# Kernel tuning notes

Measured on AMD Instinct MI355X. Metric: run time of the kernel, lower is better.

Reference implementation:

```python
import jax, jax.numpy as jnp
import numpy as np

B, C, N = 2, 512, 2048
HEADS, DIM_HEAD, SCALE = 16, 64, 8.0
H_DIM = HEADS * DIM_HEAD
EPS = 1e-12  # F.normalize default eps


def setup_inputs() -> dict:
    key = jax.random.key(0)
    ks = jax.random.split(key, 5)
    x = jax.random.normal(ks[0], (B, C, N), dtype=jnp.float32)
    Wqkv = jax.random.normal(ks[1], (3 * H_DIM, C), dtype=jnp.float32) * (1.0 / np.sqrt(C))
    q_scale = jnp.ones((DIM_HEAD,), dtype=jnp.float32)
    k_scale = jnp.ones((DIM_HEAD,), dtype=jnp.float32)
    Wout = jax.random.normal(ks[2], (C, H_DIM), dtype=jnp.float32) * (1.0 / np.sqrt(H_DIM))
    bout = jax.random.normal(ks[3], (C,), dtype=jnp.float32) * 0.01
    return {"x": x, "Wqkv": Wqkv, "q_scale": q_scale, "k_scale": k_scale,
            "Wout": Wout, "bout": bout}


def _l2norm(t):
    # F.normalize(t, dim=-1): t / max(||t||, eps)
    n = jnp.sqrt(jnp.sum(t * t, axis=-1, keepdims=True))
    return t / jnp.maximum(n, EPS)


def reference(x, Wqkv, q_scale, k_scale, Wout, bout):
    # 1x1 conv == pointwise matmul over channel dim
    qkv = jnp.einsum('oc,bcn->bon', Wqkv, x)              # [B, 3*H_DIM, N]
    q, k, v = jnp.split(qkv, 3, axis=1)
    # unflatten channels -> [B, H, D, N]
    def to_heads(t):
        return t.reshape(B, HEADS, DIM_HEAD, N)
    q, k, v = map(to_heads, (q, k, v))
    # cosine attention: l2-normalize q,k over head dim, apply learned per-dim scales
    q = _l2norm(q.transpose(0, 1, 3, 2)) * q_scale        # [B, H, N, D]
    k = _l2norm(k.transpose(0, 1, 3, 2)) * k_scale        # [B, H, N, D]
    sim = jnp.einsum('bhid,bhjd->bhij', q, k) * SCALE     # [B, H, N, N]
    attn = jax.nn.softmax(sim, axis=-1)
    out = jnp.einsum('bhij,bhdj->bhid', attn, v)          # [B, H, N, D]
    out = out.transpose(0, 1, 3, 2).reshape(B, H_DIM, N)  # b h n d -> b (h d) n
    return jnp.einsum('oc,bcn->bon', Wout, out) + bout[None, :, None]
```

## Files before the change

### kernel.cpp

```cpp
#include <hip/hip_runtime.h>
#include <hip/hip_bf16.h>

#define BATCH 2
#define CCH   512
#define NSEQ  2048
#define HEADS 16
#define DHEAD 64
#define HDIM  1024
#define ODIM  3072
#define QK_PRESCALE 11.541560327111707f

typedef short short4v __attribute__((ext_vector_type(4)));
typedef short short8 __attribute__((ext_vector_type(8)));
typedef float float4v __attribute__((ext_vector_type(4)));
typedef int   int4v   __attribute__((ext_vector_type(4)));

__device__ __forceinline__ unsigned short f2bf(float f) {
    unsigned int u = __float_as_uint(f);
    return (unsigned short)((u + 0x7FFFu + ((u >> 16) & 1u)) >> 16);
}
__device__ __forceinline__ unsigned short f2bf_fast(float f) {
    return (unsigned short)((__float_as_uint(f) + 0x8000u) >> 16);
}
__device__ __forceinline__ float fexp2(float x) {
#if __has_builtin(__builtin_amdgcn_exp2f)
    return __builtin_amdgcn_exp2f(x);
#else
    return exp2f(x);
#endif
}
__device__ __forceinline__ int pack_bf16(float lo, float hi) {
#if __has_builtin(__builtin_amdgcn_cvt_pk_bf16_f32)
    typedef __bf16 bf2_t __attribute__((ext_vector_type(2)));
    bf2_t v = __builtin_amdgcn_cvt_pk_bf16_f32(lo, hi);
    return __builtin_bit_cast(int, v);
#else
    return (int)f2bf_fast(lo) | ((int)(unsigned)f2bf_fast(hi) << 16);
#endif
}

typedef __attribute__((address_space(1))) const void* as1_cvp;
typedef __attribute__((address_space(3))) void* as3_vp;
__device__ __forceinline__ void cp16(const void* g, void* l) {
    __builtin_amdgcn_global_load_lds((as1_cvp)g, (as3_vp)l, 16, 0, 0);
}
__global__ __launch_bounds__(256) void k_prep(
    const float* __restrict__ Wqkv, const float* __restrict__ Wout,
    const float* __restrict__ x,
    const float* __restrict__ qs, const float* __restrict__ ks,
    unsigned short* __restrict__ Wqkvb, unsigned short* __restrict__ Woutb,
    unsigned short* __restrict__ xt, float* __restrict__ M) {
    const int bx = blockIdx.x;
    if (bx < 2048) {
        if (bx == 0 && threadIdx.x < 64) {
            int lane = threadIdx.x;
            float p = fabsf(qs[lane] * ks[lane]);
#pragma unroll
            for (int off = 1; off < 64; off <<= 1) p = fmaxf(p, __shfl_xor(p, off));
            if (lane == 0) *M = QK_PRESCALE * p;
        }
        int i4 = (bx * 256 + threadIdx.x) * 4;
        const float* src; unsigned short* dst; int idx;
        if (i4 < ODIM * CCH) { src = Wqkv; dst = Wqkvb; idx = i4; }
        else { src = Wout; dst = Woutb; idx = i4 - ODIM * CCH; }
        float4 v = *(const float4*)(src + idx);
        ushort4 o;
        o.x = f2bf(v.x); o.y = f2bf(v.y); o.z = f2bf(v.z); o.w = f2bf(v.w);
        *(ushort4*)(dst + idx) = o;
        return;
    }
    __shared__ unsigned short t[64][65];
    const int fx = bx - 2048;
    const int n0 = (fx & 31) * 64;
    const int c0 = ((fx >> 5) & 7) * 64;
    const int b  = fx >> 8;
    const int tr = threadIdx.x >> 6, tc = threadIdx.x & 63;
    const float* xs = x + (size_t)b * CCH * NSEQ;
    unsigned short* xd = xt + (size_t)b * NSEQ * CCH;
#pragma unroll
    for (int r = 0; r < 16; ++r) {
        int c = r * 4 + tr;
        t[c][tc] = f2bf(xs[(size_t)(c0 + c) * NSEQ + n0 + tc]);
    }
    __syncthreads();
#pragma unroll
    for (int r = 0; r < 16; ++r) {
        int n = r * 4 + tr;
        xd[(size_t)(n0 + n) * CCH + c0 + tc] = t[tc][n];
    }
}

__global__ __launch_bounds__(256) void k_gemm_qkv(
    const unsigned short* __restrict__ W, const unsigned short* __restrict__ xt,
    const float* __restrict__ qs, const float* __restrict__ ks,
    unsigned short* __restrict__ qh, unsigned short* __restrict__ kh,
    unsigned short* __restrict__ vb) {
    constexpr int K = CCH, N = NSEQ;
    __shared__ __align__(16) short smem[2 * 128 * 64];
    short* lsA = smem;
    short* lsB = smem + 128 * 64;
    const int tid = threadIdx.x, wave = tid >> 6, lane = tid & 63;
    const int l15 = lane & 15, quad = lane >> 4;
    const int n0 = blockIdx.x * 128, m0 = blockIdx.y * 128, z = blockIdx.z;
    const short* Ab = (const short*)W + (size_t)m0 * K;
    const short* Bb = (const short*)xt + ((size_t)z * N + n0) * K;
    const int wm = wave >> 1, wn = wave & 1;
    const int cswz = (((tid & 7) ^ ((tid >> 3) & 7))) * 8;
    const int sw7 = (l15 & 7);

    float4v acc[4][4];
#pragma unroll
    for (int i = 0; i < 4; ++i)
#pragma unroll
        for (int j = 0; j < 4; ++j) acc[i][j] = (float4v){0.f, 0.f, 0.f, 0.f};

    for (int k0 = 0; k0 < K; k0 += 64) {
#pragma unroll
        for (int it = 0; it < 4; ++it) {
            int row = it * 32 + (tid >> 3);
            cp16(Ab + (size_t)row * K + k0 + cswz, &lsA[it * 2048 + wave * 512]);
            cp16(Bb + (size_t)row * K + k0 + cswz, &lsB[it * 2048 + wave * 512]);
        }
        __syncthreads();
        short8 af[4][2], bfr[4][2];
#pragma unroll
        for (int t = 0; t < 4; ++t)
#pragma unroll
            for (int kk = 0; kk < 2; ++kk) {
                af[t][kk]  = *(const short8*)&lsA[(wm * 64 + t * 16 + l15) * 64 + ((kk * 4 + quad) ^ sw7) * 8];
                bfr[t][kk] = *(const short8*)&lsB[(wn * 64 + t * 16 + l15) * 64 + ((kk * 4 + quad) ^ sw7) * 8];
            }
#pragma unroll
        for (int mt = 0; mt < 4; ++mt)
#pragma unroll
            for (int nt = 0; nt < 4; ++nt) {
                acc[mt][nt] = __builtin_amdgcn_mfma_f32_16x16x32_bf16(af[mt][0], bfr[nt][0], acc[mt][nt], 0, 0, 0);
                acc[mt][nt] = __builtin_amdgcn_mfma_f32_16x16x32_bf16(af[mt][1], bfr[nt][1], acc[mt][nt], 0, 0, 0);
            }
        __syncthreads();
    }

    const int co   = (m0 + wm * 64) >> 6;
    const int part = co >> 4;
    const int h    = co & 15;
    const int bh   = z * HEADS + h;
    short* myT = smem + wave * 4096;

    if (part < 2) {
        float inv[4];
#pragma unroll
        for (int nt = 0; nt < 4; ++nt) {
            float ss = 0.f;
#pragma unroll
            for (int mt = 0; mt < 4; ++mt)
#pragma unroll
                for (int r = 0; r < 4; ++r) ss += acc[mt][nt][r] * acc[mt][nt][r];
            ss += __shfl_xor(ss, 16);
            ss += __shfl_xor(ss, 32);
            inv[nt] = 1.0f / fmaxf(sqrtf(ss), 1e-12f);
        }
        const float* sc = part ? ks : qs;
        const float csc = part ? 1.0f : QK_PRESCALE;
#pragma unroll
        for (int mt = 0; mt < 4; ++mt) {
            const int db = mt * 16 + quad * 4;
            float4 s4 = *(const float4*)(sc + db);
            s4.x *= csc; s4.y *= csc; s4.z *= csc; s4.w *= csc;
#pragma unroll
            for (int nt = 0; nt < 4; ++nt) {
                int nl = nt * 16 + l15;
                short4v o;
                o.x = (short)f2bf(acc[mt][nt][0] * inv[nt] * s4.x);
                o.y = (short)f2bf(acc[mt][nt][1] * inv[nt] * s4.y);
                o.z = (short)f2bf(acc[mt][nt][2] * inv[nt] * s4.z);
                o.w = (short)f2bf(acc[mt][nt][3] * inv[nt] * s4.w);
                *(short4v*)&myT[nl * 64 + (((db >> 3) ^ (nl & 7)) << 3) + (db & 7)] = o;
            }
        }
        unsigned short* dst = (part ? kh : qh) + (size_t)bh * NSEQ * DHEAD
                              + (size_t)(n0 + wn * 64) * DHEAD;
#pragma unroll
        for (int pass = 0; pass < 8; ++pass) {
            int nl = pass * 8 + (lane >> 3), c = lane & 7;
            short8 vv = *(const short8*)&myT[nl * 64 + ((c ^ (nl & 7)) << 3)];
            *(short8*)&dst[(size_t)nl * DHEAD + c * 8] = vv;
        }
    } else {
#pragma unroll
        for (int mt = 0; mt < 4; ++mt)
#pragma unroll
            for (int nt = 0; nt < 4; ++nt) {
                int nl = nt * 16 + l15;
                int swc = nl >> 3, swo = nl & 7;
#pragma unroll
                for (int r = 0; r < 4; ++r) {
                    int d = mt * 16 + quad * 4 + r;
                    myT[d * 64 + ((swc ^ (d & 7)) << 3) + swo] = (short)f2bf(acc[mt][nt][r]);
                }
            }
        unsigned short* dst = vb + (size_t)bh * DHEAD * NSEQ + n0 + wn * 64;
#pragma unroll
        for (int pass = 0; pass < 8; ++pass) {
            int d = pass * 8 + (lane >> 3), c = lane & 7;
            short8 vv = *(const short8*)&myT[d * 64 + ((c ^ (d & 7)) << 3)];
            *(short8*)&dst[(size_t)d * NSEQ + c * 8] = vv;
        }
    }
}

__global__ __launch_bounds__(512, 4) void k_attn(
    const unsigned short* __restrict__ qh, const unsigned short* __restrict__ kh,
    const unsigned short* __restrict__ vb,
    unsigned short* __restrict__ aot, const float* __restrict__ Mptr) {
    __shared__ __align__(16) short Kt[2][2][64 * 64];
    __shared__ __align__(16) short Vt[2][2][64 * 64];
    const int tid = threadIdx.x, wave = tid >> 6, lane = tid & 63;
    const int grp = wave >> 2, w4 = wave & 3;
    const int gtid = tid & 255;
    const int l15 = lane & 15, quad = lane >> 4, q8 = quad * 8;
    const int flat = blockIdx.x;
    const int xcd = flat & 7, idx = flat >> 3;
    const int bh = xcd * 4 + (idx >> 4);
    const int i0 = (idx & 15) * 128;
    const int b = bh >> 4, h = bh & 15;
    const float Ms = *Mptr;
    const float4v mInit = (float4v){-Ms, -Ms, -Ms, -Ms};
    const int srow = gtid >> 3;
    const int kkey  = (srow & 3) | (((srow >> 3) & 1) << 2);
    const int cswzK = ((gtid & 7) ^ kkey) * 8;
    const int cswzV = ((gtid & 7) ^ (srow & 7)) * 8;
    const int ksw = l15 & 7;
    const int kc0 = ((0 + quad) ^ ksw) * 8;
    const int kc1 = ((4 + quad) ^ ksw) * 8;
    const int ar0 = (l15 >> 2) * 8 + (l15 & 3);
    const int ar1 = ar0 + 4;
    const int jbase = grp * (NSEQ / 2);

    short8 qf[2][2];
    {
        const short* qb = (const short*)qh + ((size_t)bh * NSEQ + i0 + w4 * 32) * DHEAD;
#pragma unroll
        for (int it = 0; it < 2; ++it) {
            qf[it][0] = *(const short8*)&qb[(it * 16 + l15) * DHEAD + q8];
            qf[it][1] = *(const short8*)&qb[(it * 16 + l15) * DHEAD + 32 + q8];
        }
    }

    float4v of[2][4];
#pragma unroll
    for (int it = 0; it < 2; ++it)
#pragma unroll
        for (int dt = 0; dt < 4; ++dt) of[it][dt] = (float4v){0.f, 0.f, 0.f, 0.f};
    float l_acc[2] = {0.f, 0.f};

    const short* kbase = (const short*)kh + ((size_t)bh * NSEQ + jbase) * DHEAD;
    const short* vbase = (const short*)vb + (size_t)bh * DHEAD * NSEQ + jbase;

#pragma unroll
    for (int it = 0; it < 2; ++it) {
        int row = it * 32 + srow;
        cp16(kbase + (size_t)row * DHEAD + cswzK, &Kt[grp][0][it * 2048 + w4 * 512]);
        cp16(vbase + (size_t)row * NSEQ + cswzV, &Vt[grp][0][it * 2048 + w4 * 512]);
    }
    __syncthreads();

    int buf = 0;
    for (int j0 = 0; j0 < NSEQ / 2; j0 += 64) {
        if (j0 + 64 < NSEQ / 2) {
            int nb = buf ^ 1;
#pragma unroll
            for (int it = 0; it < 2; ++it) {
                int row = it * 32 + srow;
                cp16(kbase + (size_t)(j0 + 64 + row) * DHEAD + cswzK, &Kt[grp][nb][it * 2048 + w4 * 512]);
                cp16(vbase + (size_t)row * NSEQ + j0 + 64 + cswzV, &Vt[grp][nb][it * 2048 + w4 * 512]);
            }
        }

#pragma unroll
        for (int ch = 0; ch < 2; ++ch) {
            short8 av[4];
#pragma unroll
            for (int dt = 0; dt < 4; ++dt) {
                int vrow = dt * 16 + l15;
                av[dt] = *(const short8*)&Vt[grp][buf][vrow * 64 + (((ch * 4 + quad) ^ (l15 & 7))) * 8];
            }
            int4v pw[2];
#pragma unroll
            for (int t = 0; t < 2; ++t) {
                const int arow = ch * 32 + (t ? ar1 : ar0);
                const short* kr = &Kt[grp][buf][arow * 64];
                short8 kf0 = *(const short8*)&kr[kc0];
                short8 kf1 = *(const short8*)&kr[kc1];
#pragma unroll
                for (int it = 0; it < 2; ++it) {
                    float4v s = mInit;
                    s = __builtin_amdgcn_mfma_f32_16x16x32_bf16(kf0, qf[it][0], s, 0, 0, 0);
                    s = __builtin_amdgcn_mfma_f32_16x16x32_bf16(kf1, qf[it][1], s, 0, 0, 0);
                    float p0 = fexp2(s[0]);
                    float p1 = fexp2(s[1]);
                    float p2 = fexp2(s[2]);
                    float p3 = fexp2(s[3]);
                    l_acc[it] += (p0 + p1) + (p2 + p3);
                    pw[it][t * 2 + 0] = pack_bf16(p0, p1);
                    pw[it][t * 2 + 1] = pack_bf16(p2, p3);
                }
            }
            short8 pb0 = __builtin_bit_cast(short8, pw[0]);
            short8 pb1 = __builtin_bit_cast(short8, pw[1]);
#pragma unroll
            for (int dt = 0; dt < 4; ++dt) {
                of[0][dt] = __builtin_amdgcn_mfma_f32_16x16x32_bf16(av[dt], pb0, of[0][dt], 0, 0, 0);
                of[1][dt] = __builtin_amdgcn_mfma_f32_16x16x32_bf16(av[dt], pb1, of[1][dt], 0, 0, 0);
            }
        }

        __syncthreads();
        buf ^= 1;
    }

    float lred[2];
#pragma unroll
    for (int it = 0; it < 2; ++it) {
        float l = l_acc[it];
        l += __shfl_xor(l, 16);
        l += __shfl_xor(l, 32);
        lred[it] = l;
    }

    float* F = (float*)&Kt[0][0][0];
    float* L = (float*)&Vt[0][0][0];
    if (grp == 1) {
#pragma unroll
        for (int it = 0; it < 2; ++it) {
#pragma unroll
            for (int dt = 0; dt < 4; ++dt)
                *(float4v*)&F[(((w4 * 2 + it) * 4 + dt) * 64 + lane) * 4] = of[it][dt];
            L[(w4 * 2 + it) * 64 + lane] = lred[it];
        }
    }
    __syncthreads();
    if (grp == 0) {
#pragma unroll
        for (int it = 0; it < 2; ++it) {
            float lt = lred[it] + L[(w4 * 2 + it) * 64 + lane];
            float inv = 1.0f / fmaxf(lt, 1e-30f);
            unsigned short* ob = aot + ((size_t)b * NSEQ + i0 + w4 * 32 + it * 16 + l15) * HDIM + h * DHEAD;
#pragma unroll
            for (int dt = 0; dt < 4; ++dt) {
                float4v p = *(const float4v*)&F[(((w4 * 2 + it) * 4 + dt) * 64 + lane) * 4];
                ushort4 o;
                o.x = f2bf((of[it][dt][0] + p[0]) * inv);
                o.y = f2bf((of[it][dt][1] + p[1]) * inv);
                o.z = f2bf((of[it][dt][2] + p[2]) * inv);
                o.w = f2bf((of[it][dt][3] + p[3]) * inv);
                *(ushort4*)&ob[dt * 16 + quad * 4] = o;
            }
        }
    }
}

__global__ __launch_bounds__(256) void k_gemm_out(
    const unsigned short* __restrict__ W, const unsigned short* __restrict__ aot,
    const float* __restrict__ bias, float* __restrict__ out) {
    constexpr int K = HDIM, N = NSEQ, M = CCH;
    __shared__ __align__(16) short lsA[64 * 64];
    __shared__ __align__(16) short lsB[64 * 64];
    const int tid = threadIdx.x, wave = tid >> 6, lane = tid & 63;
    const int l15 = lane & 15, quad = lane >> 4;
    const int n0 = blockIdx.x * 64, m0 = blockIdx.y * 64, z = blockIdx.z;
    const short* Ab = (const short*)W + (size_t)m0 * K;
    const short* Bb = (const short*)aot + ((size_t)z * N + n0) * K;
    const int wm = wave >> 1, wn = wave & 1;
    const int cswz = (((tid & 7) ^ ((tid >> 3) & 7))) * 8;
    const int sw7 = (l15 & 7);

    float4v acc[2][2];
#pragma unroll
    for (int i = 0; i < 2; ++i)
#pragma unroll
        for (int j = 0; j < 2; ++j) acc[i][j] = (float4v){0.f, 0.f, 0.f, 0.f};

    for (int k0 = 0; k0 < K; k0 += 64) {
        {
            int row = tid >> 3;
            cp16(Ab + (size_t)row * K + k0 + cswz, &lsA[wave * 512]);
            cp16(Ab + (size_t)(row + 32) * K + k0 + cswz, &lsA[2048 + wave * 512]);
            cp16(Bb + (size_t)row * K + k0 + cswz, &lsB[wave * 512]);
            cp16(Bb + (size_t)(row + 32) * K + k0 + cswz, &lsB[2048 + wave * 512]);
        }
        __syncthreads();
        short8 af[2][2], bfr[2][2];
#pragma unroll
        for (int t = 0; t < 2; ++t)
#pragma unroll
            for (int kk = 0; kk < 2; ++kk) {
                af[t][kk]  = *(const short8*)&lsA[(wm * 32 + t * 16 + l15) * 64 + ((kk * 4 + quad) ^ sw7) * 8];
                bfr[t][kk] = *(const short8*)&lsB[(wn * 32 + t * 16 + l15) * 64 + ((kk * 4 + quad) ^ sw7) * 8];
            }
#pragma unroll
        for (int mt = 0; mt < 2; ++mt)
#pragma unroll
            for (int nt = 0; nt < 2; ++nt) {
                acc[mt][nt] = __builtin_amdgcn_mfma_f32_16x16x32_bf16(af[mt][0], bfr[nt][0], acc[mt][nt], 0, 0, 0);
                acc[mt][nt] = __builtin_amdgcn_mfma_f32_16x16x32_bf16(af[mt][1], bfr[nt][1], acc[mt][nt], 0, 0, 0);
            }
        __syncthreads();
    }
    float* Co = out + (size_t)z * M * N;
#pragma unroll
    for (int mt = 0; mt < 2; ++mt)
#pragma unroll
        for (int nt = 0; nt < 2; ++nt) {
            int mrow = m0 + wm * 32 + mt * 16 + quad * 4;
#pragma unroll
            for (int r = 0; r < 4; ++r) {
                int mr = mrow + r;
                int nc = n0 + wn * 32 + nt * 16 + l15;
                Co[(size_t)mr * N + nc] = acc[mt][nt][r] + bias[mr];
            }
        }
}

extern "C" void kernel_launch(void* const* d_in, const int* in_sizes, int n_in,
                              void* d_out, int out_size, void* d_ws, size_t ws_size,
                              hipStream_t stream) {
    const float* x = nullptr; const float* Wqkv = nullptr;
    const float* qs = nullptr; const float* ks = nullptr;
    const float* Wout = nullptr; const float* bout = nullptr;
    for (int i = 0; i < n_in; ++i) {
        switch (in_sizes[i]) {
            case BATCH * CCH * NSEQ: x    = (const float*)d_in[i]; break;
            case ODIM * CCH:         Wqkv = (const float*)d_in[i]; break;
            case CCH * HDIM:         Wout = (const float*)d_in[i]; break;
            case CCH:                bout = (const float*)d_in[i]; break;
            case DHEAD: if (!qs) qs = (const float*)d_in[i]; else ks = (const float*)d_in[i]; break;
            default: break;
        }
    }
    float* y = (float*)d_out;

    char* ws = (char*)d_ws;
    float*          Mbuf  = (float*)(ws + 0);
    unsigned short* Wqkvb = (unsigned short*)(ws + 4096);
    unsigned short* Woutb = (unsigned short*)(ws + 3149824);
    unsigned short* xt    = (unsigned short*)(ws + 4198400);
    unsigned short* qh    = (unsigned short*)(ws + 8392704);
    unsigned short* kh    = (unsigned short*)(ws + 16781312);
    unsigned short* vb    = (unsigned short*)(ws + 25169920);
    unsigned short* aot   = (unsigned short*)(ws + 33558528);

    k_prep<<<dim3(2048 + 512), 256, 0, stream>>>(Wqkv, Wout, x, qs, ks, Wqkvb, Woutb, xt, Mbuf);
    k_gemm_qkv<<<dim3(NSEQ / 128, ODIM / 128, BATCH), 256, 0, stream>>>(Wqkvb, xt, qs, ks, qh, kh, vb);
    k_attn<<<dim3(512), 512, 0, stream>>>(qh, kh, vb, aot, Mbuf);
    k_gemm_out<<<dim3(NSEQ / 64, CCH / 64, BATCH), 256, 0, stream>>>(Woutb, aot, bout, y);
}
```

Measured before the change: 150.0 us.

## Pipeline attention K/V loads with 4-stage ring and single barrier per tile

```diff
diff --git a/kernel.cpp b/kernel.cpp
--- a/kernel.cpp
+++ b/kernel.cpp
@@ -208,12 +208,13 @@
     }
 }
 
+#define KVB 32
 __global__ __launch_bounds__(512, 4) void k_attn(
     const unsigned short* __restrict__ qh, const unsigned short* __restrict__ kh,
     const unsigned short* __restrict__ vb,
     unsigned short* __restrict__ aot, const float* __restrict__ Mptr) {
-    __shared__ __align__(16) short Kt[2][2][64 * 64];
-    __shared__ __align__(16) short Vt[2][2][64 * 64];
+    __shared__ __align__(16) short Kt[2][4][KVB * 64];
+    __shared__ __align__(16) short Vt[2][4][64 * KVB];
     const int tid = threadIdx.x, wave = tid >> 6, lane = tid & 63;
     const int grp = wave >> 2, w4 = wave & 3;
     const int gtid = tid & 255;
@@ -225,13 +226,15 @@
     const int b = bh >> 4, h = bh & 15;
     const float Ms = *Mptr;
     const float4v mInit = (float4v){-Ms, -Ms, -Ms, -Ms};
-    const int srow = gtid >> 3;
-    const int kkey  = (srow & 3) | (((srow >> 3) & 1) << 2);
+    const int srowK = gtid >> 3;
+    const int kkey  = (srowK & 3) | (((srowK >> 3) & 1) << 2);
     const int cswzK = ((gtid & 7) ^ kkey) * 8;
-    const int cswzV = ((gtid & 7) ^ (srow & 7)) * 8;
+    const int srowV = gtid >> 2;
+    const int cswzV = ((gtid & 3) ^ ((srowV >> 1) & 3)) * 8;
     const int ksw = l15 & 7;
     const int kc0 = ((0 + quad) ^ ksw) * 8;
     const int kc1 = ((4 + quad) ^ ksw) * 8;
+    const int vkr = (l15 >> 1) & 3;
     const int ar0 = (l15 >> 2) * 8 + (l15 & 3);
     const int ar1 = ar0 + 4;
     const int jbase = grp * (NSEQ / 2);
@@ -256,67 +259,74 @@
     const short* kbase = (const short*)kh + ((size_t)bh * NSEQ + jbase) * DHEAD;
     const short* vbase = (const short*)vb + (size_t)bh * DHEAD * NSEQ + jbase;
 
-#pragma unroll
-    for (int it = 0; it < 2; ++it) {
-        int row = it * 32 + srow;
-        cp16(kbase + (size_t)row * DHEAD + cswzK, &Kt[grp][0][it * 2048 + w4 * 512]);
-        cp16(vbase + (size_t)row * NSEQ + cswzV, &Vt[grp][0][it * 2048 + w4 * 512]);
-    }
-    __syncthreads();
-
-    int buf = 0;
-    for (int j0 = 0; j0 < NSEQ / 2; j0 += 64) {
-        if (j0 + 64 < NSEQ / 2) {
-            int nb = buf ^ 1;
-#pragma unroll
-            for (int it = 0; it < 2; ++it) {
-                int row = it * 32 + srow;
-                cp16(kbase + (size_t)(j0 + 64 + row) * DHEAD + cswzK, &Kt[grp][nb][it * 2048 + w4 * 512]);
-                cp16(vbase + (size_t)row * NSEQ + j0 + 64 + cswzV, &Vt[grp][nb][it * 2048 + w4 * 512]);
-            }
-        }
-
-#pragma unroll
-        for (int ch = 0; ch < 2; ++ch) {
-            short8 av[4];
-#pragma unroll
-            for (int dt = 0; dt < 4; ++dt) {
-                int vrow = dt * 16 + l15;
-                av[dt] = *(const short8*)&Vt[grp][buf][vrow * 64 + (((ch * 4 + quad) ^ (l15 & 7))) * 8];
-            }
-            int4v pw[2];
-#pragma unroll
-            for (int t = 0; t < 2; ++t) {
-                const int arow = ch * 32 + (t ? ar1 : ar0);
-                const short* kr = &Kt[grp][buf][arow * 64];
-                short8 kf0 = *(const short8*)&kr[kc0];
-                short8 kf1 = *(const short8*)&kr[kc1];
-#pragma unroll
-                for (int it = 0; it < 2; ++it) {
-                    float4v s = mInit;
-                    s = __builtin_amdgcn_mfma_f32_16x16x32_bf16(kf0, qf[it][0], s, 0, 0, 0);
-                    s = __builtin_amdgcn_mfma_f32_16x16x32_bf16(kf1, qf[it][1], s, 0, 0, 0);
-                    float p0 = fexp2(s[0]);
-                    float p1 = fexp2(s[1]);
-                    float p2 = fexp2(s[2]);
-                    float p3 = fexp2(s[3]);
-                    l_acc[it] += (p0 + p1) + (p2 + p3);
-                    pw[it][t * 2 + 0] = pack_bf16(p0, p1);
-                    pw[it][t * 2 + 1] = pack_bf16(p2, p3);
-                }
-            }
-            short8 pb0 = __builtin_bit_cast(short8, pw[0]);
-            short8 pb1 = __builtin_bit_cast(short8, pw[1]);
-#pragma unroll
-            for (int dt = 0; dt < 4; ++dt) {
-                of[0][dt] = __builtin_amdgcn_mfma_f32_16x16x32_bf16(av[dt], pb0, of[0][dt], 0, 0, 0);
-                of[1][dt] = __builtin_amdgcn_mfma_f32_16x16x32_bf16(av[dt], pb1, of[1][dt], 0, 0, 0);
-            }
-        }
-
-        __syncthreads();
-        buf ^= 1;
-    }
+#define STAGE(T_, B_) do {                                                       \
+        cp16(kbase + (size_t)((T_) * KVB + srowK) * DHEAD + cswzK,               \
+             &Kt[grp][B_][w4 * 512]);                                            \
+        cp16(vbase + (size_t)srowV * NSEQ + (T_) * KVB + cswzV,                  \
+             &Vt[grp][B_][w4 * 512]);                                            \
+    } while (0)
+
+#define COMPUTE(CB_) do {                                                        \
+        const short* Kb = &Kt[grp][CB_][0];                                      \
+        const short* Vb = &Vt[grp][CB_][0];                                      \
+        __builtin_amdgcn_s_setprio(1);                                           \
+        short8 av[4];                                                            \
+        _Pragma("unroll")                                                        \
+        for (int dt = 0; dt < 4; ++dt)                                           \
+            av[dt] = *(const short8*)&Vb[(dt * 16 + l15) * KVB + ((quad ^ vkr) * 8)]; \
+        int4v pw[2];                                                             \
+        _Pragma("unroll")                                                        \
+        for (int t2 = 0; t2 < 2; ++t2) {                                         \
+            const int arow = t2 ? ar1 : ar0;                                     \
+            const short* kr = &Kb[arow * 64];                                    \
+            short8 kf0 = *(const short8*)&kr[kc0];                               \
+            short8 kf1 = *(const short8*)&kr[kc1];                               \
+            _Pragma("unroll")                                                    \
+            for (int it = 0; it < 2; ++it) {                                     \
+                float4v s = mInit;                                               \
+                s = __builtin_amdgcn_mfma_f32_16x16x32_bf16(kf0, qf[it][0], s, 0, 0, 0); \
+                s = __builtin_amdgcn_mfma_f32_16x16x32_bf16(kf1, qf[it][1], s, 0, 0, 0); \
+                float p0 = fexp2(s[0]);                                          \
+                float p1 = fexp2(s[1]);                                          \
+                float p2 = fexp2(s[2]);                                          \
+                float p3 = fexp2(s[3]);                                          \
+                l_acc[it] += (p0 + p1) + (p2 + p3);                              \
+                pw[it][t2 * 2 + 0] = pack_bf16(p0, p1);                          \
+                pw[it][t2 * 2 + 1] = pack_bf16(p2, p3);                          \
+            }                                                                    \
+        }                                                                        \
+        {                                                                        \
+            short8 pb0 = __builtin_bit_cast(short8, pw[0]);                      \
+            short8 pb1 = __builtin_bit_cast(short8, pw[1]);                      \
+            _Pragma("unroll")                                                    \
+            for (int dt = 0; dt < 4; ++dt) {                                     \
+                of[0][dt] = __builtin_amdgcn_mfma_f32_16x16x32_bf16(av[dt], pb0, of[0][dt], 0, 0, 0); \
+                of[1][dt] = __builtin_amdgcn_mfma_f32_16x16x32_bf16(av[dt], pb1, of[1][dt], 0, 0, 0); \
+            }                                                                    \
+        }                                                                        \
+        __builtin_amdgcn_s_setprio(0);                                           \
+    } while (0)
+
+    constexpr int T = (NSEQ / 2) / KVB;
+    STAGE(0, 0);
+    STAGE(1, 1);
+    for (int t = 0; t < T - 2; ++t) {
+        STAGE(t + 2, (t + 2) & 3);
+        asm volatile("s_waitcnt vmcnt(4)" ::: "memory");
+        __builtin_amdgcn_s_barrier();
+        __builtin_amdgcn_sched_barrier(0);
+        COMPUTE(t & 3);
+    }
+    asm volatile("s_waitcnt vmcnt(2)" ::: "memory");
+    __builtin_amdgcn_s_barrier();
+    __builtin_amdgcn_sched_barrier(0);
+    COMPUTE((T - 2) & 3);
+    asm volatile("s_waitcnt vmcnt(0)" ::: "memory");
+    __builtin_amdgcn_s_barrier();
+    __builtin_amdgcn_sched_barrier(0);
+    COMPUTE((T - 1) & 3);
+#undef STAGE
+#undef COMPUTE
 
     float lred[2];
 #pragma unroll
@@ -326,6 +336,8 @@
         l += __shfl_xor(l, 32);
         lred[it] = l;
     }
+
+    __syncthreads();
 
     float* F = (float*)&Kt[0][0][0];
     float* L = (float*)&Vt[0][0][0];
```

After: 149.1 us. Within noise of the previous version (-0.6%).
